# Performance work log

Hardware: AMD Instinct MI355X
Metric: run time of the kernel (lower is better)

## Reference

```python
import jax, jax.numpy as jnp
import numpy as np

NEG = jnp.float32(-1e30)  # log-space 'zero' (safer than -inf under jit/grad)
ALPHA = 0.5
GAMMA = 2.0
BLANK = 0


def _ctc_loss_mean(log_probs, targets, input_lengths, target_lengths):
    # log_probs: [T, N, C] (already log-softmaxed), targets: [N, S] (labels >= 1)
    T, N, C = log_probs.shape
    S = targets.shape[1]
    L = 2 * S + 1  # extended target: blank-interleaved

    # extended targets: even positions = blank, odd = labels
    ext = jnp.zeros((N, L), dtype=jnp.int32).at[:, 1::2].set(targets.astype(jnp.int32))
    l_idx = jnp.arange(L)
    valid = l_idx[None, :] < (2 * target_lengths + 1)[:, None]  # [N, L]
    ext_m2 = jnp.pad(ext, ((0, 0), (2, 0)))[:, :L]
    can_skip = (l_idx[None, :] >= 2) & (ext != BLANK) & (ext != ext_m2)  # [N, L]

    # gather per-frame log-probs of extended labels: [T, N, L] (small lattice)
    lp_ext = jnp.take_along_axis(log_probs, jnp.broadcast_to(ext[None], (T, N, L)), axis=2)

    # alpha at t=0
    alpha0 = jnp.full((N, L), NEG)
    alpha0 = alpha0.at[:, 0].set(lp_ext[0, :, 0]).at[:, 1].set(lp_ext[0, :, 1])
    alpha0 = jnp.where(valid, alpha0, NEG)

    def step(alpha, x):
        lp_t, t = x
        a1 = alpha
        a2 = jnp.pad(alpha, ((0, 0), (1, 0)), constant_values=NEG)[:, :L]
        a3 = jnp.where(can_skip, jnp.pad(alpha, ((0, 0), (2, 0)), constant_values=NEG)[:, :L], NEG)
        m = jnp.maximum(jnp.maximum(a1, a2), a3)
        new = m + jnp.log(jnp.exp(a1 - m) + jnp.exp(a2 - m) + jnp.exp(a3 - m)) + lp_t
        new = jnp.where(valid, new, NEG)
        # freeze alpha once past this sample's input length
        alpha = jnp.where((t < input_lengths)[:, None], new, alpha)
        return alpha, None

    alphaT, _ = jax.lax.scan(step, alpha0, (lp_ext[1:], jnp.arange(1, T)))

    i1 = (2 * target_lengths)[:, None]
    i2 = (2 * target_lengths - 1)[:, None]
    a1 = jnp.take_along_axis(alphaT, i1, axis=1)[:, 0]
    a2 = jnp.take_along_axis(alphaT, i2, axis=1)[:, 0]
    loss = -jnp.logaddexp(a1, a2)  # [N]
    # zero_infinity=True: infeasible alignments -> 0
    loss = jnp.where(loss > 1e29, 0.0, loss)
    # reduction='mean': divide by target lengths, then mean over batch
    return jnp.mean(loss / target_lengths.astype(loss.dtype))


def setup_inputs() -> dict:
    key = jax.random.key(0)
    k1, k2, k3 = jax.random.split(key, 3)
    T, N, C, S = 160, 128, 6625, 32
    log_probs = jax.nn.log_softmax(jax.random.normal(k1, (T, N, C), dtype=jnp.float32), axis=-1)
    targets = jax.random.randint(k2, (N, S), 1, C).astype(jnp.int32)  # labels exclude blank=0
    input_lengths = jnp.full((N,), T, dtype=jnp.int32)
    target_lengths = jax.random.randint(k3, (N,), 16, S + 1).astype(jnp.int32)
    return {"log_probs": log_probs, "targets": targets,
            "input_lengths": input_lengths, "target_lengths": target_lengths}


def reference(log_probs, targets, input_lengths, target_lengths):
    loss_ctc = _ctc_loss_mean(log_probs, targets, input_lengths, target_lengths)
    p = jnp.exp(-loss_ctc)
    return ALPHA * (1.0 - p) ** GAMMA * loss_ctc
```

## Files before the change

### kernel.cpp

```cpp
#include <hip/hip_runtime.h>
#include <math.h>


#define TT 160
#define NN 128
#define CC 6625
#define SS 32
#define JJ 33
#define NEGV  (-1e30f)
#define LOG2E 1.4426950408889634f
#define LN2   0.6931471805599453f

__device__ __forceinline__ float dpp_up1(float x, bool row0lane) {
    int xi = __float_as_int(x);
    int shr = __builtin_amdgcn_update_dpp(xi, xi, 0x111, 0xf, 0xf, false);
    int bc  = __builtin_amdgcn_update_dpp(xi, xi, 0x142, 0xf, 0xf, false);
    return __int_as_float(row0lane ? bc : shr);
}

__global__ __launch_bounds__(1024) void ctc_fused_kernel(
    const float* __restrict__ log_probs,
    const int*   __restrict__ targets,
    const int*   __restrict__ input_lengths,
    const int*   __restrict__ target_lengths,
    float*       __restrict__ per_sample)
{
    const int n   = blockIdx.x;
    const int tid = threadIdx.x;

    __shared__ float lp[TT * JJ];
    __shared__ int   lab[JJ];

    if (tid < JJ) lab[tid] = (tid == 0) ? 0 : targets[n * SS + tid - 1];
    __syncthreads();

    const size_t rowbase = (size_t)n * CC;
#pragma unroll
    for (int k = 0; k < 6; ++k) {
        const int i = tid + k * 1024;
        if (i < TT * JJ) {
            const int t = i / JJ;
            const int j = i - t * JJ;
            lp[i] = log_probs[(size_t)t * (NN * CC) + rowbase + lab[j]] * LOG2E;
        }
    }
    __syncthreads();

    if (tid >= 64) return;
    const int lane = tid;

    const int tl = target_lengths[n];
    const int Lv = 2 * tl + 1;
    const int slot = (lane & 1) ? (1 + (lane >> 1)) : 0;
    const bool skip = (lane & 1) && (lane >= 3) &&
                      (lab[1 + (lane >> 1)] != lab[lane >> 1]);
    const bool validl  = lane < Lv;
    const bool valid64 = 64 < Lv;
    const bool row0lane = (lane & 15) == 0;

    float v = NEGV;
    if (lane == 0) v = lp[0];
    if (lane == 1) v = lp[1];
    float e = NEGV;

    const int ilen = input_lengths[n];
    const int Tlim = (ilen < TT) ? ilen : TT;

    for (int t = 1; t < Tlim; ++t) {
        const float u1 = dpp_up1(v, row0lane);
        const float u2 = dpp_up1(u1, row0lane);
        const float a2 = (lane == 0) ? NEGV : u1;
        const float a3 = skip ? u2 : NEGV;

        const float lpt64 = lp[t * JJ];
        const float me = fmaxf(e, v);
        const float ne = me + log2f(exp2f(e - me) + exp2f(v - me)) + lpt64;

        const float m  = fmaxf(v, fmaxf(a2, a3));
        const float nv = m + log2f(exp2f(v - m) + exp2f(a2 - m) + exp2f(a3 - m))
                           + lp[t * JJ + slot];

        v = validl  ? nv : NEGV;
        e = valid64 ? ne : NEGV;
    }

    const int i1 = 2 * tl;
    const int i2 = 2 * tl - 1;
    const float A1 = (i1 == 64) ? __shfl(e, 63) : __shfl(v, i1);
    const float A2 = __shfl(v, i2);
    if (lane == 0) {
        const float m = fmaxf(A1, A2);
        float loss = -LN2 * (m + log2f(exp2f(A1 - m) + exp2f(A2 - m)));
        if (loss > 1e29f) loss = 0.0f;
        per_sample[n] = loss / (float)tl;
    }
}

__global__ __launch_bounds__(128) void focal_reduce_kernel(
    const float* __restrict__ per_sample, float* __restrict__ out)
{
    __shared__ float s[NN];
    int tid = threadIdx.x;
    s[tid] = per_sample[tid];
    __syncthreads();
    for (int off = NN / 2; off > 0; off >>= 1) {
        if (tid < off) s[tid] += s[tid + off];
        __syncthreads();
    }
    if (tid == 0) {
        float mean = s[0] / (float)NN;
        float pp = expf(-mean);
        float om = 1.0f - pp;
        out[0] = 0.5f * om * om * mean;
    }
}

extern "C" void kernel_launch(void* const* d_in, const int* in_sizes, int n_in,
                              void* d_out, int out_size, void* d_ws, size_t ws_size,
                              hipStream_t stream) {
    const float* log_probs      = (const float*)d_in[0];
    const int*   targets        = (const int*)d_in[1];
    const int*   input_lengths  = (const int*)d_in[2];
    const int*   target_lengths = (const int*)d_in[3];
    float* out        = (float*)d_out;
    float* per_sample = (float*)d_ws;

    ctc_fused_kernel<<<NN, 1024, 0, stream>>>(log_probs, targets, input_lengths,
                                              target_lengths, per_sample);
    focal_reduce_kernel<<<1, NN, 0, stream>>>(per_sample, out);
}
```

Baseline: 48.31 us.

## Split per-sample gather across four blocks with spin-flag handoff to leader

Measured after the change: 86.73 us. 79.5% more time.

```diff
diff --git a/kernel.cpp b/kernel.cpp
--- a/kernel.cpp
+++ b/kernel.cpp
@@ -7,6 +7,8 @@
 #define CC 6625
 #define SS 32
 #define JJ 33
+#define NTJ (TT * JJ)
+#define QTR 1320
 #define NEGV  (-1e30f)
 #define LOG2E 1.4426950408889634f
 #define LN2   0.6931471805599453f
@@ -18,31 +20,64 @@
     return __int_as_float(row0lane ? bc : shr);
 }
 
-__global__ __launch_bounds__(1024) void ctc_fused_kernel(
+__global__ __launch_bounds__(128) void clear_flags(int* __restrict__ flags) {
+    flags[threadIdx.x] = 0;
+}
+
+__global__ __launch_bounds__(512) void ctc_spin_kernel(
     const float* __restrict__ log_probs,
     const int*   __restrict__ targets,
     const int*   __restrict__ input_lengths,
     const int*   __restrict__ target_lengths,
+    int*         __restrict__ flags,
+    float*       __restrict__ lp_ws,
     float*       __restrict__ per_sample)
 {
-    const int n   = blockIdx.x;
+    const int bid = blockIdx.x;
+    const int n   = bid >> 2;
+    const int q   = bid & 3;
     const int tid = threadIdx.x;
 
-    __shared__ float lp[TT * JJ];
+    __shared__ float lp[NTJ];
     __shared__ int   lab[JJ];
 
     if (tid < JJ) lab[tid] = (tid == 0) ? 0 : targets[n * SS + tid - 1];
     __syncthreads();
 
+    float* wsn = lp_ws + (size_t)n * NTJ;
     const size_t rowbase = (size_t)n * CC;
 #pragma unroll
-    for (int k = 0; k < 6; ++k) {
-        const int i = tid + k * 1024;
-        if (i < TT * JJ) {
+    for (int k = 0; k < 3; ++k) {
+        const int i = q * QTR + tid + k * 512;
+        if (i < (q + 1) * QTR) {
             const int t = i / JJ;
             const int j = i - t * JJ;
-            lp[i] = log_probs[(size_t)t * (NN * CC) + rowbase + lab[j]] * LOG2E;
+            const float val = log_probs[(size_t)t * (NN * CC) + rowbase + lab[j]] * LOG2E;
+            if (q == 0) lp[i] = val;
+            else        wsn[i] = val;
         }
+    }
+    __syncthreads();
+
+    if (q != 0) {
+        if (tid == 0) { __threadfence(); atomicAdd(&flags[n], 1); }
+        return;
+    }
+
+    if (tid == 0) {
+        while (__hip_atomic_load(&flags[n], __ATOMIC_ACQUIRE,
+                                 __HIP_MEMORY_SCOPE_AGENT) < 3)
+            __builtin_amdgcn_s_sleep(1);
+        __threadfence();
+    }
+    __syncthreads();
+
+    const float4* s4 = (const float4*)wsn;
+    float4* d4 = (float4*)lp;
+#pragma unroll
+    for (int k = 0; k < 2; ++k) {
+        const int i = QTR / 4 + tid + k * 512;
+        if (i < NTJ / 4) d4[i] = s4[i];
     }
     __syncthreads();
 
@@ -54,8 +89,8 @@
     const int slot = (lane & 1) ? (1 + (lane >> 1)) : 0;
     const bool skip = (lane & 1) && (lane >= 3) &&
                       (lab[1 + (lane >> 1)] != lab[lane >> 1]);
-    const bool validl  = lane < Lv;
-    const bool valid64 = 64 < Lv;
+    const bool validl   = lane < Lv;
+    const bool valid64  = 64 < Lv;
     const bool row0lane = (lane & 15) == 0;
 
     float v = NEGV;
@@ -122,10 +157,15 @@
     const int*   targets        = (const int*)d_in[1];
     const int*   input_lengths  = (const int*)d_in[2];
     const int*   target_lengths = (const int*)d_in[3];
-    float* out        = (float*)d_out;
-    float* per_sample = (float*)d_ws;
+    float* out = (float*)d_out;
 
-    ctc_fused_kernel<<<NN, 1024, 0, stream>>>(log_probs, targets, input_lengths,
-                                              target_lengths, per_sample);
+    int*   flags      = (int*)d_ws;
+    float* per_sample = (float*)((char*)d_ws + 2048);
+    float* lp_ws      = (float*)((char*)d_ws + 4096);
+
+    clear_flags<<<1, 128, 0, stream>>>(flags);
+    ctc_spin_kernel<<<NN * 4, 512, 0, stream>>>(log_probs, targets,
+                                                input_lengths, target_lengths,
+                                                flags, lp_ws, per_sample);
     focal_reduce_kernel<<<1, NN, 0, stream>>>(per_sample, out);
 }
```

## Overlap chunked log-prob gather with alpha recursion across waves

Applied to the files above, without the earlier changes.

Result: faster. 39.66 us (-17.9%).

```diff
diff --git a/kernel.cpp b/kernel.cpp
--- a/kernel.cpp
+++ b/kernel.cpp
@@ -7,6 +7,10 @@
 #define CC 6625
 #define SS 32
 #define JJ 33
+#define NTJ (TT * JJ)
+#define CHT 32
+#define CHE (CHT * JJ)
+#define NCH 5
 #define NEGV  (-1e30f)
 #define LOG2E 1.4426950408889634f
 #define LN2   0.6931471805599453f
@@ -28,17 +32,18 @@
     const int n   = blockIdx.x;
     const int tid = threadIdx.x;
 
-    __shared__ float lp[TT * JJ];
+    __shared__ float lp[NTJ];
     __shared__ int   lab[JJ];
 
     if (tid < JJ) lab[tid] = (tid == 0) ? 0 : targets[n * SS + tid - 1];
     __syncthreads();
 
     const size_t rowbase = (size_t)n * CC;
+
 #pragma unroll
-    for (int k = 0; k < 6; ++k) {
+    for (int k = 0; k < 2; ++k) {
         const int i = tid + k * 1024;
-        if (i < TT * JJ) {
+        if (i < CHE) {
             const int t = i / JJ;
             const int j = i - t * JJ;
             lp[i] = log_probs[(size_t)t * (NN * CC) + rowbase + lab[j]] * LOG2E;
@@ -46,16 +51,15 @@
     }
     __syncthreads();
 
-    if (tid >= 64) return;
     const int lane = tid;
-
     const int tl = target_lengths[n];
     const int Lv = 2 * tl + 1;
     const int slot = (lane & 1) ? (1 + (lane >> 1)) : 0;
     const bool skip = (lane & 1) && (lane >= 3) &&
-                      (lab[1 + (lane >> 1)] != lab[lane >> 1]);
-    const bool validl  = lane < Lv;
-    const bool valid64 = 64 < Lv;
+                      (lab[(lane >> 1) < SS ? 1 + (lane >> 1) : 1] !=
+                       lab[(lane >> 1) < 1 ? 0 : (lane >> 1)]);
+    const bool validl   = lane < Lv;
+    const bool valid64  = 64 < Lv;
     const bool row0lane = (lane & 15) == 0;
 
     float v = NEGV;
@@ -66,23 +70,46 @@
     const int ilen = input_lengths[n];
     const int Tlim = (ilen < TT) ? ilen : TT;
 
-    for (int t = 1; t < Tlim; ++t) {
-        const float u1 = dpp_up1(v, row0lane);
-        const float u2 = dpp_up1(u1, row0lane);
-        const float a2 = (lane == 0) ? NEGV : u1;
-        const float a3 = skip ? u2 : NEGV;
+    for (int c = 0; c < NCH; ++c) {
+        if (tid >= 64 && c + 1 < NCH) {
+            const int base = (c + 1) * CHE;
+#pragma unroll
+            for (int k = 0; k < 2; ++k) {
+                const int r = (tid - 64) + k * 960;
+                if (r < CHE) {
+                    const int i = base + r;
+                    const int t = i / JJ;
+                    const int j = i - t * JJ;
+                    lp[i] = log_probs[(size_t)t * (NN * CC) + rowbase + lab[j]] * LOG2E;
+                }
+            }
+        }
+        if (tid < 64) {
+            const int t_lo = (c == 0) ? 1 : c * CHT;
+            int t_hi = (c + 1) * CHT;
+            if (t_hi > Tlim) t_hi = Tlim;
+            for (int t = t_lo; t < t_hi; ++t) {
+                const float u1 = dpp_up1(v, row0lane);
+                const float u2 = dpp_up1(u1, row0lane);
+                const float a2 = (lane == 0) ? NEGV : u1;
+                const float a3 = skip ? u2 : NEGV;
 
-        const float lpt64 = lp[t * JJ];
-        const float me = fmaxf(e, v);
-        const float ne = me + log2f(exp2f(e - me) + exp2f(v - me)) + lpt64;
+                const float lpt64 = lp[t * JJ];
+                const float me = fmaxf(e, v);
+                const float ne = me + log2f(exp2f(e - me) + exp2f(v - me)) + lpt64;
 
-        const float m  = fmaxf(v, fmaxf(a2, a3));
-        const float nv = m + log2f(exp2f(v - m) + exp2f(a2 - m) + exp2f(a3 - m))
-                           + lp[t * JJ + slot];
+                const float m  = fmaxf(v, fmaxf(a2, a3));
+                const float nv = m + log2f(exp2f(v - m) + exp2f(a2 - m) + exp2f(a3 - m))
+                                   + lp[t * JJ + slot];
 
-        v = validl  ? nv : NEGV;
-        e = valid64 ? ne : NEGV;
+                v = validl  ? nv : NEGV;
+                e = valid64 ? ne : NEGV;
+            }
+        }
+        __syncthreads();
     }
+
+    if (tid >= 64) return;
 
     const int i1 = 2 * tl;
     const int i2 = 2 * tl - 1;
```
